# Kernel tuning notes

Measured on AMD Instinct MI355X. Metric: run time of the kernel, lower is better.

Reference implementation:

```python
import jax, jax.numpy as jnp
import numpy as np

B, S, D = 2, 4096, 1024
EPS = 1e-05


def setup_inputs() -> dict:
    key = jax.random.key(0)
    ks = jax.random.split(key, 7)
    x = jax.random.normal(ks[0], (B, S, D), dtype=jnp.float32)
    gamma = jnp.ones((D,), dtype=jnp.float32)
    wq, wk, wv, wa, wg, wo = (jax.random.normal(k, (D, D), dtype=jnp.float32) for k in ks[1:7])
    return {"x": x, "gamma": gamma, "wq": wq, "wk": wk, "wv": wv, "wa": wa, "wg": wg, "wo": wo}


def _rmsnorm(x, gamma):
    # original uses sum of squares (not mean) with scale = sqrt(dim)
    ss = jnp.sum(jnp.square(x), axis=-1, keepdims=True)
    inv = jax.lax.rsqrt(ss + EPS)
    return inv * x * gamma * (x.shape[-1] ** 0.5)


def _gate_loop_operator(kv, q, a):
    def binop(e_i, e_j):
        a_i, kv_i = e_i
        a_j, kv_j = e_j
        return (a_j * a_i, a_j * kv_i + kv_j)
    _, y = jax.lax.associative_scan(binop, (a, kv), axis=1)
    return q * y


def reference(x, gamma, wq, wk, wv, wa, wg, wo):
    x = _rmsnorm(x, gamma)
    q = x @ wq
    k = x @ wk
    v = x @ wv
    a = jax.nn.sigmoid(x @ wa)
    g = x @ wg
    kv = k * v
    y = _gate_loop_operator(kv, q, a)
    y = y * jax.nn.silu(g)
    return y @ wo
```

## Files before the change

### kernel.cpp

```cpp
#include <hip/hip_runtime.h>
#include <hip/hip_bf16.h>
#include <cstdint>
#include <cstddef>


typedef __bf16 bf16x8 __attribute__((ext_vector_type(8)));
typedef float f32x4 __attribute__((ext_vector_type(4)));

__device__ __forceinline__ void gload_lds16(const void* g, void* l) {
  __builtin_amdgcn_global_load_lds(
      (const __attribute__((address_space(1))) void*)g,
      (__attribute__((address_space(3))) void*)l,
      16, 0, 0);
}

__global__ __launch_bounds__(256) void wconv_k(
    const float* __restrict__ wq, const float* __restrict__ wk,
    const float* __restrict__ wv, const float* __restrict__ wa,
    const float* __restrict__ wg, const float* __restrict__ wo,
    __hip_bfloat16* __restrict__ wcatT, __hip_bfloat16* __restrict__ woT) {
  __shared__ float t[32][33];
  const float* src;
  __hip_bfloat16* dst;
  switch (blockIdx.z) {
    case 0: src = wq; dst = wcatT; break;
    case 1: src = wk; dst = wcatT + (size_t)1024 * 1024; break;
    case 2: src = wv; dst = wcatT + (size_t)2048 * 1024; break;
    case 3: src = wg; dst = wcatT + (size_t)3072 * 1024; break;
    case 4: src = wa; dst = wcatT + (size_t)4096 * 1024; break;
    default: src = wo; dst = woT; break;
  }
  const int n0 = blockIdx.x * 32;
  const int k0 = blockIdx.y * 32;
  const int tx = threadIdx.x, ty = threadIdx.y;
#pragma unroll
  for (int i = 0; i < 32; i += 8)
    t[ty + i][tx] = src[(size_t)(k0 + ty + i) * 1024 + n0 + tx];
  __syncthreads();
#pragma unroll
  for (int i = 0; i < 32; i += 8)
    dst[(size_t)(n0 + ty + i) * 1024 + k0 + tx] = __float2bfloat16(t[tx][ty + i]);
}

__global__ __launch_bounds__(256) void rmsnorm_k(
    const float* __restrict__ x, const float* __restrict__ gamma,
    __hip_bfloat16* __restrict__ xn) {
  const int row = blockIdx.x;
  const int tid = threadIdx.x;
  const float4 xv = ((const float4*)(x + (size_t)row * 1024))[tid];
  float ss = xv.x * xv.x + xv.y * xv.y + xv.z * xv.z + xv.w * xv.w;
#pragma unroll
  for (int off = 32; off >= 1; off >>= 1) ss += __shfl_xor(ss, off, 64);
  __shared__ float wss[4];
  if ((tid & 63) == 0) wss[tid >> 6] = ss;
  __syncthreads();
  const float total = wss[0] + wss[1] + wss[2] + wss[3];
  const float scale = rsqrtf(total + 1e-5f) * 32.0f;
  const float4 gv = ((const float4*)gamma)[tid];
  union { __hip_bfloat16 h[4]; ushort4 u; } ob;
  ob.h[0] = __float2bfloat16(xv.x * gv.x * scale);
  ob.h[1] = __float2bfloat16(xv.y * gv.y * scale);
  ob.h[2] = __float2bfloat16(xv.z * gv.z * scale);
  ob.h[3] = __float2bfloat16(xv.w * gv.w * scale);
  ((ushort4*)(xn + (size_t)row * 1024))[tid] = ob.u;
}

__global__ __launch_bounds__(512, 2) void gemm256(
    const __hip_bfloat16* __restrict__ A, const __hip_bfloat16* __restrict__ Bt,
    int M, int N, int K,
    __hip_bfloat16* __restrict__ outb, int ldb, int nbcols,
    float* __restrict__ outf, int ldf) {
  __shared__ __align__(16) unsigned short As[4 * 8192];
  __shared__ __align__(16) unsigned short Bs[4 * 8192];

  const int tid = threadIdx.x;
  const int nwg = gridDim.x * gridDim.y;
  const int bid = blockIdx.y * gridDim.x + blockIdx.x;
  const int swz = (bid & 7) * (nwg >> 3) + (bid >> 3);
  const int brow = (swz / gridDim.x) * 256;
  const int bcol = (swz % gridDim.x) * 256;

  const unsigned short* Ag = (const unsigned short*)A + (size_t)brow * K;
  const unsigned short* Bg = (const unsigned short*)Bt + (size_t)bcol * K;

  const int srow = tid >> 2;
  const int sch8 = (((tid & 3) ^ ((srow >> 1) & 3)) << 3);

  auto stageA = [&](int sl) {
    unsigned short* dst = As + ((sl & 3) << 13);
    const int k0 = sl << 5;
    gload_lds16(Ag + (size_t)srow * K + k0 + sch8, dst + tid * 8);
    gload_lds16(Ag + (size_t)(srow + 128) * K + k0 + sch8, dst + 4096 + tid * 8);
  };
  auto stageB = [&](int sl) {
    unsigned short* dst = Bs + ((sl & 3) << 13);
    const int k0 = sl << 5;
    gload_lds16(Bg + (size_t)srow * K + k0 + sch8, dst + tid * 8);
    gload_lds16(Bg + (size_t)(srow + 128) * K + k0 + sch8, dst + 4096 + tid * 8);
  };

  const int lane = tid & 63;
  const int wid = tid >> 6;
  const int wr = wid >> 2;
  const int wc = wid & 3;
  const int l16 = lane & 15;
  const int k8 = lane >> 4;

  int aoff[8], boff[4];
#pragma unroll
  for (int m = 0; m < 8; ++m) {
    const int r = wr * 128 + m * 16 + l16;
    aoff[m] = r * 32 + ((k8 ^ ((r >> 1) & 3)) << 3);
  }
#pragma unroll
  for (int n = 0; n < 4; ++n) {
    const int r = wc * 64 + n * 16 + l16;
    boff[n] = r * 32 + ((k8 ^ ((r >> 1) & 3)) << 3);
  }

  f32x4 acc[8][4];
#pragma unroll
  for (int m = 0; m < 8; ++m)
#pragma unroll
    for (int n = 0; n < 4; ++n) acc[m][n] = (f32x4){0.f, 0.f, 0.f, 0.f};

  const int NS = K >> 5;
  stageA(0); stageB(0);
  stageA(1); stageB(1);
  stageA(2); stageB(2);
  asm volatile("s_waitcnt vmcnt(8)" ::: "memory");
  __builtin_amdgcn_s_barrier();

  for (int s = 0; s < NS; ++s) {
    const unsigned short* As_s = As + ((s & 3) << 13);
    const unsigned short* Bs_s = Bs + ((s & 3) << 13);
    bf16x8 af[8], bfr[4];
#pragma unroll
    for (int m = 0; m < 8; ++m) af[m] = *(const bf16x8*)(As_s + aoff[m]);
    bfr[0] = *(const bf16x8*)(Bs_s + boff[0]);
    bfr[1] = *(const bf16x8*)(Bs_s + boff[1]);
    if (s + 3 < NS) stageA(s + 3);
    __builtin_amdgcn_s_barrier();
    __builtin_amdgcn_s_setprio(1);
#pragma unroll
    for (int m = 0; m < 8; ++m) {
      acc[m][0] = __builtin_amdgcn_mfma_f32_16x16x32_bf16(af[m], bfr[0], acc[m][0], 0, 0, 0);
      acc[m][1] = __builtin_amdgcn_mfma_f32_16x16x32_bf16(af[m], bfr[1], acc[m][1], 0, 0, 0);
    }
    __builtin_amdgcn_s_setprio(0);
    __builtin_amdgcn_s_barrier();
    bfr[2] = *(const bf16x8*)(Bs_s + boff[2]);
    bfr[3] = *(const bf16x8*)(Bs_s + boff[3]);
    if (s + 3 < NS) stageB(s + 3);
    __builtin_amdgcn_s_barrier();
    __builtin_amdgcn_s_setprio(1);
#pragma unroll
    for (int m = 0; m < 8; ++m) {
      acc[m][2] = __builtin_amdgcn_mfma_f32_16x16x32_bf16(af[m], bfr[2], acc[m][2], 0, 0, 0);
      acc[m][3] = __builtin_amdgcn_mfma_f32_16x16x32_bf16(af[m], bfr[3], acc[m][3], 0, 0, 0);
    }
    __builtin_amdgcn_s_setprio(0);
    if (s < NS - 3)       asm volatile("s_waitcnt vmcnt(8)" ::: "memory");
    else if (s == NS - 3) asm volatile("s_waitcnt vmcnt(4)" ::: "memory");
    else if (s == NS - 2) asm volatile("s_waitcnt vmcnt(0)" ::: "memory");
    __builtin_amdgcn_s_barrier();
  }

  const int mb = brow + wr * 128 + k8 * 4;
  const int nb = bcol + wc * 64 + l16;
#pragma unroll
  for (int m = 0; m < 8; ++m) {
#pragma unroll
    for (int n = 0; n < 4; ++n) {
      const int col = nb + n * 16;
#pragma unroll
      for (int r = 0; r < 4; ++r) {
        const int row = mb + m * 16 + r;
        const float v = acc[m][n][r];
        if (col < nbcols) {
          outb[(size_t)row * ldb + col] = __float2bfloat16(v);
        } else {
          outf[(size_t)row * ldf + (col - nbcols)] = v;
        }
      }
    }
  }
}

__global__ __launch_bounds__(256) void scan_pass1(
    const __hip_bfloat16* __restrict__ qkvg, const float* __restrict__ apre,
    float* __restrict__ Asum, float* __restrict__ Ysum) {
  const int bc = blockIdx.x;
  const int d = blockIdx.y * 256 + threadIdx.x;
  const size_t rowbase = (size_t)(bc >> 5) * 4096 + (size_t)(bc & 31) * 128;
  float y = 0.f, Ap = 1.f;
  for (int s = 0; s < 128; ++s) {
    const size_t r = rowbase + s;
    const float kk = __bfloat162float(qkvg[r * 4096 + 1024 + d]);
    const float vv = __bfloat162float(qkvg[r * 4096 + 2048 + d]);
    const float ap = apre[r * 1024 + d];
    const float a = 1.f / (1.f + __expf(-ap));
    y = fmaf(a, y, kk * vv);
    Ap *= a;
  }
  Asum[(size_t)bc * 1024 + d] = Ap;
  Ysum[(size_t)bc * 1024 + d] = y;
}

__global__ __launch_bounds__(256) void scan_pass2(
    const float* __restrict__ Asum, const float* __restrict__ Ysum,
    float* __restrict__ carry) {
  const int idx = blockIdx.x * 256 + threadIdx.x;
  const int b = idx >> 10, d = idx & 1023;
  float y = 0.f;
  for (int c = 0; c < 32; ++c) {
    const size_t o = (size_t)(b * 32 + c) * 1024 + d;
    carry[o] = y;
    y = fmaf(Asum[o], y, Ysum[o]);
  }
}

__global__ __launch_bounds__(256) void scan_pass3(
    const __hip_bfloat16* __restrict__ qkvg, const float* __restrict__ apre,
    const float* __restrict__ carry, __hip_bfloat16* __restrict__ yact) {
  const int bc = blockIdx.x;
  const int d = blockIdx.y * 256 + threadIdx.x;
  const size_t rowbase = (size_t)(bc >> 5) * 4096 + (size_t)(bc & 31) * 128;
  float y = carry[(size_t)bc * 1024 + d];
  for (int s = 0; s < 128; ++s) {
    const size_t r = rowbase + s;
    const float qq = __bfloat162float(qkvg[r * 4096 + d]);
    const float kk = __bfloat162float(qkvg[r * 4096 + 1024 + d]);
    const float vv = __bfloat162float(qkvg[r * 4096 + 2048 + d]);
    const float gg = __bfloat162float(qkvg[r * 4096 + 3072 + d]);
    const float ap = apre[r * 1024 + d];
    const float a = 1.f / (1.f + __expf(-ap));
    y = fmaf(a, y, kk * vv);
    const float sg = 1.f / (1.f + __expf(-gg));
    yact[r * 1024 + d] = __float2bfloat16(qq * y * gg * sg);
  }
}

extern "C" void kernel_launch(void* const* d_in, const int* in_sizes, int n_in,
                              void* d_out, int out_size, void* d_ws, size_t ws_size,
                              hipStream_t stream) {
  const float* x     = (const float*)d_in[0];
  const float* gamma = (const float*)d_in[1];
  const float* wq    = (const float*)d_in[2];
  const float* wk    = (const float*)d_in[3];
  const float* wv    = (const float*)d_in[4];
  const float* wa    = (const float*)d_in[5];
  const float* wg    = (const float*)d_in[6];
  const float* wo    = (const float*)d_in[7];
  float* out = (float*)d_out;

  char* ws = (char*)d_ws;
  __hip_bfloat16* wcatT = (__hip_bfloat16*)(ws);
  __hip_bfloat16* woT   = (__hip_bfloat16*)(ws + 10485760);
  __hip_bfloat16* xn    = (__hip_bfloat16*)(ws + 12582912);
  __hip_bfloat16* qkvg  = (__hip_bfloat16*)(ws + 29360128);
  float*          apre  = (float*)(ws + 96468992);
  __hip_bfloat16* yact  = (__hip_bfloat16*)(ws + 130023424);
  float*          Asum  = (float*)(ws + 146800640);
  float*          Ysum  = (float*)(ws + 147062784);
  float*          carry = (float*)(ws + 147324928);

  wconv_k<<<dim3(32, 32, 6), dim3(32, 8, 1), 0, stream>>>(wq, wk, wv, wa, wg, wo, wcatT, woT);
  rmsnorm_k<<<dim3(8192), dim3(256), 0, stream>>>(x, gamma, xn);
  gemm256<<<dim3(20, 32), dim3(512), 0, stream>>>(
      xn, wcatT, 8192, 5120, 1024, qkvg, 4096, 4096, apre, 1024);
  scan_pass1<<<dim3(64, 4), dim3(256), 0, stream>>>(qkvg, apre, Asum, Ysum);
  scan_pass2<<<dim3(8), dim3(256), 0, stream>>>(Asum, Ysum, carry);
  scan_pass3<<<dim3(64, 4), dim3(256), 0, stream>>>(qkvg, apre, carry, yact);
  gemm256<<<dim3(4, 32), dim3(512), 0, stream>>>(
      yact, woT, 8192, 1024, 1024, (__hip_bfloat16*)nullptr, 0, 0, out, 1024);
}
```

Before: 220.6 us.

## Restructure GEMM main loop with fewer barriers and add 256x128 tile output GEMM

The main GEMM loop now loads all B and A fragments up front, issues both next-stage prefetches, and runs all 32 MFMAs in one block with a single barrier per K-step instead of three. The launch-bounds occupancy hint of 2 is dropped, giving the compiler more registers. A new gemm_n128 kernel with 256x128 tiles is used for the final output projection, doubling its grid from 128 to 256 workgroups to better fill the CUs on a 1024-wide output. Risks include higher register pressure and LDS bank contention from the merged loads, and a possible race since a stage buffer may be refilled while other waves are still reading it.

```diff
diff --git a/kernel.cpp b/kernel.cpp
--- a/kernel.cpp
+++ b/kernel.cpp
@@ -65,7 +65,7 @@
   ((ushort4*)(xn + (size_t)row * 1024))[tid] = ob.u;
 }
 
-__global__ __launch_bounds__(512, 2) void gemm256(
+__global__ __launch_bounds__(512) void gemm256(
     const __hip_bfloat16* __restrict__ A, const __hip_bfloat16* __restrict__ Bt,
     int M, int N, int K,
     __hip_bfloat16* __restrict__ outb, int ldb, int nbcols,
@@ -136,29 +136,19 @@
     const unsigned short* Bs_s = Bs + ((s & 3) << 13);
     bf16x8 af[8], bfr[4];
 #pragma unroll
-    for (int m = 0; m < 8; ++m) af[m] = *(const bf16x8*)(As_s + aoff[m]);
-    bfr[0] = *(const bf16x8*)(Bs_s + boff[0]);
-    bfr[1] = *(const bf16x8*)(Bs_s + boff[1]);
+    for (int n = 0; n < 4; ++n) bfr[n] = *(const bf16x8*)(Bs_s + boff[n]);
+#pragma unroll
+    for (int m = 0; m < 4; ++m) af[m] = *(const bf16x8*)(As_s + aoff[m]);
     if (s + 3 < NS) stageA(s + 3);
-    __builtin_amdgcn_s_barrier();
+#pragma unroll
+    for (int m = 4; m < 8; ++m) af[m] = *(const bf16x8*)(As_s + aoff[m]);
+    if (s + 3 < NS) stageB(s + 3);
     __builtin_amdgcn_s_setprio(1);
 #pragma unroll
-    for (int m = 0; m < 8; ++m) {
-      acc[m][0] = __builtin_amdgcn_mfma_f32_16x16x32_bf16(af[m], bfr[0], acc[m][0], 0, 0, 0);
-      acc[m][1] = __builtin_amdgcn_mfma_f32_16x16x32_bf16(af[m], bfr[1], acc[m][1], 0, 0, 0);
-    }
-    __builtin_amdgcn_s_setprio(0);
-    __builtin_amdgcn_s_barrier();
-    bfr[2] = *(const bf16x8*)(Bs_s + boff[2]);
-    bfr[3] = *(const bf16x8*)(Bs_s + boff[3]);
-    if (s + 3 < NS) stageB(s + 3);
-    __builtin_amdgcn_s_barrier();
-    __builtin_amdgcn_s_setprio(1);
-#pragma unroll
-    for (int m = 0; m < 8; ++m) {
-      acc[m][2] = __builtin_amdgcn_mfma_f32_16x16x32_bf16(af[m], bfr[2], acc[m][2], 0, 0, 0);
-      acc[m][3] = __builtin_amdgcn_mfma_f32_16x16x32_bf16(af[m], bfr[3], acc[m][3], 0, 0, 0);
-    }
+    for (int m = 0; m < 8; ++m)
+#pragma unroll
+      for (int n = 0; n < 4; ++n)
+        acc[m][n] = __builtin_amdgcn_mfma_f32_16x16x32_bf16(af[m], bfr[n], acc[m][n], 0, 0, 0);
     __builtin_amdgcn_s_setprio(0);
     if (s < NS - 3)       asm volatile("s_waitcnt vmcnt(8)" ::: "memory");
     else if (s == NS - 3) asm volatile("s_waitcnt vmcnt(4)" ::: "memory");
@@ -182,6 +172,110 @@
         } else {
           outf[(size_t)row * ldf + (col - nbcols)] = v;
         }
+      }
+    }
+  }
+}
+
+__global__ __launch_bounds__(512) void gemm_n128(
+    const __hip_bfloat16* __restrict__ A, const __hip_bfloat16* __restrict__ Bt,
+    int M, int N, int K, float* __restrict__ outf, int ldf) {
+  __shared__ __align__(16) unsigned short As[4 * 8192];
+  __shared__ __align__(16) unsigned short Bs[4 * 4096];
+
+  const int tid = threadIdx.x;
+  const int nwg = gridDim.x * gridDim.y;
+  const int bid = blockIdx.y * gridDim.x + blockIdx.x;
+  const int swz = (bid & 7) * (nwg >> 3) + (bid >> 3);
+  const int brow = (swz / gridDim.x) * 256;
+  const int bcol = (swz % gridDim.x) * 128;
+
+  const unsigned short* Ag = (const unsigned short*)A + (size_t)brow * K;
+  const unsigned short* Bg = (const unsigned short*)Bt + (size_t)bcol * K;
+
+  const int srow = tid >> 2;
+  const int sch8 = (((tid & 3) ^ ((srow >> 1) & 3)) << 3);
+
+  auto stageA = [&](int sl) {
+    unsigned short* dst = As + ((sl & 3) << 13);
+    const int k0 = sl << 5;
+    gload_lds16(Ag + (size_t)srow * K + k0 + sch8, dst + tid * 8);
+    gload_lds16(Ag + (size_t)(srow + 128) * K + k0 + sch8, dst + 4096 + tid * 8);
+  };
+  auto stageB = [&](int sl) {
+    unsigned short* dst = Bs + ((sl & 3) << 12);
+    const int k0 = sl << 5;
+    gload_lds16(Bg + (size_t)srow * K + k0 + sch8, dst + tid * 8);
+  };
+
+  const int lane = tid & 63;
+  const int wid = tid >> 6;
+  const int wr = wid >> 2;
+  const int wc = wid & 3;
+  const int l16 = lane & 15;
+  const int k8 = lane >> 4;
+
+  int aoff[8], boff[2];
+#pragma unroll
+  for (int m = 0; m < 8; ++m) {
+    const int r = wr * 128 + m * 16 + l16;
+    aoff[m] = r * 32 + ((k8 ^ ((r >> 1) & 3)) << 3);
+  }
+#pragma unroll
+  for (int n = 0; n < 2; ++n) {
+    const int r = wc * 32 + n * 16 + l16;
+    boff[n] = r * 32 + ((k8 ^ ((r >> 1) & 3)) << 3);
+  }
+
+  f32x4 acc[8][2];
+#pragma unroll
+  for (int m = 0; m < 8; ++m)
+#pragma unroll
+    for (int n = 0; n < 2; ++n) acc[m][n] = (f32x4){0.f, 0.f, 0.f, 0.f};
+
+  const int NS = K >> 5;
+  stageA(0); stageB(0);
+  stageA(1); stageB(1);
+  stageA(2); stageB(2);
+  asm volatile("s_waitcnt vmcnt(6)" ::: "memory");
+  __builtin_amdgcn_s_barrier();
+
+  for (int s = 0; s < NS; ++s) {
+    const unsigned short* As_s = As + ((s & 3) << 13);
+    const unsigned short* Bs_s = Bs + ((s & 3) << 12);
+    bf16x8 af[8], bfr[2];
+    bfr[0] = *(const bf16x8*)(Bs_s + boff[0]);
+    bfr[1] = *(const bf16x8*)(Bs_s + boff[1]);
+#pragma unroll
+    for (int m = 0; m < 4; ++m) af[m] = *(const bf16x8*)(As_s + aoff[m]);
+    if (s + 3 < NS) stageA(s + 3);
+#pragma unroll
+    for (int m = 4; m < 8; ++m) af[m] = *(const bf16x8*)(As_s + aoff[m]);
+    if (s + 3 < NS) stageB(s + 3);
+    __builtin_amdgcn_s_setprio(1);
+#pragma unroll
+    for (int m = 0; m < 8; ++m)
+#pragma unroll
+      for (int n = 0; n < 2; ++n)
+        acc[m][n] = __builtin_amdgcn_mfma_f32_16x16x32_bf16(af[m], bfr[n], acc[m][n], 0, 0, 0);
+    __builtin_amdgcn_s_setprio(0);
+    if (s < NS - 3)       asm volatile("s_waitcnt vmcnt(6)" ::: "memory");
+    else if (s == NS - 3) asm volatile("s_waitcnt vmcnt(3)" ::: "memory");
+    else if (s == NS - 2) asm volatile("s_waitcnt vmcnt(0)" ::: "memory");
+    __builtin_amdgcn_s_barrier();
+  }
+
+  const int mb = brow + wr * 128 + k8 * 4;
+  const int nb = bcol + wc * 32 + l16;
+#pragma unroll
+  for (int m = 0; m < 8; ++m) {
+#pragma unroll
+    for (int n = 0; n < 2; ++n) {
+      const int col = nb + n * 16;
+#pragma unroll
+      for (int r = 0; r < 4; ++r) {
+        const int row = mb + m * 16 + r;
+        outf[(size_t)row * ldf + col] = acc[m][n][r];
       }
     }
   }
@@ -272,6 +366,6 @@
   scan_pass1<<<dim3(64, 4), dim3(256), 0, stream>>>(qkvg, apre, Asum, Ysum);
   scan_pass2<<<dim3(8), dim3(256), 0, stream>>>(Asum, Ysum, carry);
   scan_pass3<<<dim3(64, 4), dim3(256), 0, stream>>>(qkvg, apre, carry, yact);
-  gemm256<<<dim3(4, 32), dim3(512), 0, stream>>>(
-      yact, woT, 8192, 1024, 1024, (__hip_bfloat16*)nullptr, 0, 0, out, 1024);
-}
+  gemm_n128<<<dim3(8, 32), dim3(512), 0, stream>>>(
+      yact, woT, 8192, 1024, 1024, out, 1024);
+}
```

Measured after the change: 217.7 us. Within noise of the previous version (-1.3%).

## Replace 256x256 GEMM tiles with 128x128 tiles and triple-buffered pipeline

Applied to the files above, without the earlier changes.

Shrinks the GEMM block tile from 256x256 with 8 waves to 128x128 with 4 waves. It also moves from a 4-slot split A/B staging scheme to a 3-slot combined stage with one barrier per k-step. The aim is more workgroups for better CU fill on the small output GEMM (128 tiles before, 512 after) and lower LDS and register pressure. The cost is less data reuse per tile and more global traffic. The swizzled-chunk index used when staging was also changed to match the new row mapping.

```diff
diff --git a/kernel.cpp b/kernel.cpp
--- a/kernel.cpp
+++ b/kernel.cpp
@@ -65,51 +65,48 @@
   ((ushort4*)(xn + (size_t)row * 1024))[tid] = ob.u;
 }
 
-__global__ __launch_bounds__(512, 2) void gemm256(
+__global__ __launch_bounds__(256) void gemm128(
     const __hip_bfloat16* __restrict__ A, const __hip_bfloat16* __restrict__ Bt,
     int M, int N, int K,
     __hip_bfloat16* __restrict__ outb, int ldb, int nbcols,
     float* __restrict__ outf, int ldf) {
-  __shared__ __align__(16) unsigned short As[4 * 8192];
-  __shared__ __align__(16) unsigned short Bs[4 * 8192];
+  __shared__ __align__(16) unsigned short As[3 * 4096];
+  __shared__ __align__(16) unsigned short Bs[3 * 4096];
 
   const int tid = threadIdx.x;
   const int nwg = gridDim.x * gridDim.y;
   const int bid = blockIdx.y * gridDim.x + blockIdx.x;
   const int swz = (bid & 7) * (nwg >> 3) + (bid >> 3);
-  const int brow = (swz / gridDim.x) * 256;
-  const int bcol = (swz % gridDim.x) * 256;
+  const int brow = (swz / gridDim.x) * 128;
+  const int bcol = (swz % gridDim.x) * 128;
 
   const unsigned short* Ag = (const unsigned short*)A + (size_t)brow * K;
   const unsigned short* Bg = (const unsigned short*)Bt + (size_t)bcol * K;
 
   const int srow = tid >> 2;
-  const int sch8 = (((tid & 3) ^ ((srow >> 1) & 3)) << 3);
-
-  auto stageA = [&](int sl) {
-    unsigned short* dst = As + ((sl & 3) << 13);
+  const int gch8 = (((tid & 3) ^ ((tid >> 3) & 3)) << 3);
+
+  auto stageAB = [&](int sl, int slot) {
+    unsigned short* dA = As + slot * 4096;
+    unsigned short* dB = Bs + slot * 4096;
     const int k0 = sl << 5;
-    gload_lds16(Ag + (size_t)srow * K + k0 + sch8, dst + tid * 8);
-    gload_lds16(Ag + (size_t)(srow + 128) * K + k0 + sch8, dst + 4096 + tid * 8);
-  };
-  auto stageB = [&](int sl) {
-    unsigned short* dst = Bs + ((sl & 3) << 13);
-    const int k0 = sl << 5;
-    gload_lds16(Bg + (size_t)srow * K + k0 + sch8, dst + tid * 8);
-    gload_lds16(Bg + (size_t)(srow + 128) * K + k0 + sch8, dst + 4096 + tid * 8);
+    gload_lds16(Ag + (size_t)srow * K + k0 + gch8, dA + tid * 8);
+    gload_lds16(Ag + (size_t)(srow + 64) * K + k0 + gch8, dA + 2048 + tid * 8);
+    gload_lds16(Bg + (size_t)srow * K + k0 + gch8, dB + tid * 8);
+    gload_lds16(Bg + (size_t)(srow + 64) * K + k0 + gch8, dB + 2048 + tid * 8);
   };
 
   const int lane = tid & 63;
   const int wid = tid >> 6;
-  const int wr = wid >> 2;
-  const int wc = wid & 3;
+  const int wr = wid >> 1;
+  const int wc = wid & 1;
   const int l16 = lane & 15;
   const int k8 = lane >> 4;
 
-  int aoff[8], boff[4];
-#pragma unroll
-  for (int m = 0; m < 8; ++m) {
-    const int r = wr * 128 + m * 16 + l16;
+  int aoff[4], boff[4];
+#pragma unroll
+  for (int m = 0; m < 4; ++m) {
+    const int r = wr * 64 + m * 16 + l16;
     aoff[m] = r * 32 + ((k8 ^ ((r >> 1) & 3)) << 3);
   }
 #pragma unroll
@@ -118,58 +115,50 @@
     boff[n] = r * 32 + ((k8 ^ ((r >> 1) & 3)) << 3);
   }
 
-  f32x4 acc[8][4];
-#pragma unroll
-  for (int m = 0; m < 8; ++m)
+  f32x4 acc[4][4];
+#pragma unroll
+  for (int m = 0; m < 4; ++m)
 #pragma unroll
     for (int n = 0; n < 4; ++n) acc[m][n] = (f32x4){0.f, 0.f, 0.f, 0.f};
 
   const int NS = K >> 5;
-  stageA(0); stageB(0);
-  stageA(1); stageB(1);
-  stageA(2); stageB(2);
-  asm volatile("s_waitcnt vmcnt(8)" ::: "memory");
+  stageAB(0, 0);
+  stageAB(1, 1);
+  asm volatile("s_waitcnt vmcnt(4)" ::: "memory");
   __builtin_amdgcn_s_barrier();
 
+  int rs = 0, ws = 2;
   for (int s = 0; s < NS; ++s) {
-    const unsigned short* As_s = As + ((s & 3) << 13);
-    const unsigned short* Bs_s = Bs + ((s & 3) << 13);
-    bf16x8 af[8], bfr[4];
-#pragma unroll
-    for (int m = 0; m < 8; ++m) af[m] = *(const bf16x8*)(As_s + aoff[m]);
-    bfr[0] = *(const bf16x8*)(Bs_s + boff[0]);
-    bfr[1] = *(const bf16x8*)(Bs_s + boff[1]);
-    if (s + 3 < NS) stageA(s + 3);
-    __builtin_amdgcn_s_barrier();
+    if (s + 2 < NS) stageAB(s + 2, ws);
+    const unsigned short* As_s = As + rs * 4096;
+    const unsigned short* Bs_s = Bs + rs * 4096;
+    bf16x8 af[4], bfr[4];
+#pragma unroll
+    for (int m = 0; m < 4; ++m) af[m] = *(const bf16x8*)(As_s + aoff[m]);
+#pragma unroll
+    for (int n = 0; n < 4; ++n) bfr[n] = *(const bf16x8*)(Bs_s + boff[n]);
     __builtin_amdgcn_s_setprio(1);
 #pragma unroll
-    for (int m = 0; m < 8; ++m) {
-      acc[m][0] = __builtin_amdgcn_mfma_f32_16x16x32_bf16(af[m], bfr[0], acc[m][0], 0, 0, 0);
-      acc[m][1] = __builtin_amdgcn_mfma_f32_16x16x32_bf16(af[m], bfr[1], acc[m][1], 0, 0, 0);
+    for (int m = 0; m < 4; ++m)
+#pragma unroll
+      for (int n = 0; n < 4; ++n)
+        acc[m][n] = __builtin_amdgcn_mfma_f32_16x16x32_bf16(af[m], bfr[n], acc[m][n], 0, 0, 0);
+    __builtin_amdgcn_s_setprio(0);
+    if (s <= NS - 3) {
+      asm volatile("s_waitcnt vmcnt(4)" ::: "memory");
+      __builtin_amdgcn_s_barrier();
+    } else if (s == NS - 2) {
+      asm volatile("s_waitcnt vmcnt(0)" ::: "memory");
+      __builtin_amdgcn_s_barrier();
     }
-    __builtin_amdgcn_s_setprio(0);
-    __builtin_amdgcn_s_barrier();
-    bfr[2] = *(const bf16x8*)(Bs_s + boff[2]);
-    bfr[3] = *(const bf16x8*)(Bs_s + boff[3]);
-    if (s + 3 < NS) stageB(s + 3);
-    __builtin_amdgcn_s_barrier();
-    __builtin_amdgcn_s_setprio(1);
-#pragma unroll
-    for (int m = 0; m < 8; ++m) {
-      acc[m][2] = __builtin_amdgcn_mfma_f32_16x16x32_bf16(af[m], bfr[2], acc[m][2], 0, 0, 0);
-      acc[m][3] = __builtin_amdgcn_mfma_f32_16x16x32_bf16(af[m], bfr[3], acc[m][3], 0, 0, 0);
-    }
-    __builtin_amdgcn_s_setprio(0);
-    if (s < NS - 3)       asm volatile("s_waitcnt vmcnt(8)" ::: "memory");
-    else if (s == NS - 3) asm volatile("s_waitcnt vmcnt(4)" ::: "memory");
-    else if (s == NS - 2) asm volatile("s_waitcnt vmcnt(0)" ::: "memory");
-    __builtin_amdgcn_s_barrier();
-  }
-
-  const int mb = brow + wr * 128 + k8 * 4;
+    rs = (rs == 2) ? 0 : rs + 1;
+    ws = (ws == 2) ? 0 : ws + 1;
+  }
+
+  const int mb = brow + wr * 64 + k8 * 4;
   const int nb = bcol + wc * 64 + l16;
 #pragma unroll
-  for (int m = 0; m < 8; ++m) {
+  for (int m = 0; m < 4; ++m) {
 #pragma unroll
     for (int n = 0; n < 4; ++n) {
       const int col = nb + n * 16;
@@ -267,11 +256,11 @@
 
   wconv_k<<<dim3(32, 32, 6), dim3(32, 8, 1), 0, stream>>>(wq, wk, wv, wa, wg, wo, wcatT, woT);
   rmsnorm_k<<<dim3(8192), dim3(256), 0, stream>>>(x, gamma, xn);
-  gemm256<<<dim3(20, 32), dim3(512), 0, stream>>>(
+  gemm128<<<dim3(40, 64), dim3(256), 0, stream>>>(
       xn, wcatT, 8192, 5120, 1024, qkvg, 4096, 4096, apre, 1024);
   scan_pass1<<<dim3(64, 4), dim3(256), 0, stream>>>(qkvg, apre, Asum, Ysum);
   scan_pass2<<<dim3(8), dim3(256), 0, stream>>>(Asum, Ysum, carry);
   scan_pass3<<<dim3(64, 4), dim3(256), 0, stream>>>(qkvg, apre, carry, yact);
-  gemm256<<<dim3(4, 32), dim3(512), 0, stream>>>(
+  gemm128<<<dim3(8, 64), dim3(256), 0, stream>>>(
       yact, woT, 8192, 1024, 1024, (__hip_bfloat16*)nullptr, 0, 0, out, 1024);
 }
```

Result: no change. 222.8 us (+1.0%).
